# Optimization experiments

Measured on AMD Instinct MI355X. Metric: run time of the kernel, lower is better.

## Reference

```python
import jax, jax.numpy as jnp
import numpy as np

N = 100000
E = 1600000
D_IN = 128
D_H = 256


def setup_inputs() -> dict:
    key = jax.random.key(0)
    ks = jax.random.split(key, 8)
    x = jax.random.normal(ks[0], (N, D_IN), dtype=jnp.float32)
    x_tilde = jax.random.normal(ks[1], (N, D_IN), dtype=jnp.float32)
    adj_row = jnp.sort(jax.random.randint(ks[2], (E,), 0, N, dtype=jnp.int32))
    adj_col = jax.random.randint(ks[3], (E,), 0, N, dtype=jnp.int32)
    # normalized-ish positive edge weights
    adj_vals = jax.random.uniform(ks[4], (E,), dtype=jnp.float32) / 16.0
    # Linear weight (torch layout [out, in]), xavier-ish scale
    W1 = jax.random.normal(ks[5], (D_H, D_IN), dtype=jnp.float32) * (2.0 / (D_IN + D_H)) ** 0.5
    prelu_a = jnp.full((1,), 0.25, dtype=jnp.float32)  # PReLU default slope
    w_bil = jax.random.normal(ks[6], (D_H, D_H), dtype=jnp.float32) * (2.0 / (2 * D_H)) ** 0.5
    return {"x": x, "x_tilde": x_tilde, "adj_vals": adj_vals, "adj_row": adj_row,
            "adj_col": adj_col, "W1": W1, "prelu_a": prelu_a, "w_bil": w_bil}


def reference(x, x_tilde, adj_vals, adj_row, adj_col, W1, prelu_a, w_bil):
    n = x.shape[0]

    def gcn(feat):
        # SpMM: agg[r] = sum_e vals[e] * feat[col[e]] for edges with row[e]==r
        gathered = adj_vals[:, None] * feat[adj_col]  # [E, D_IN]
        agg = jax.ops.segment_sum(gathered, adj_row, num_segments=n)  # [N, D_IN]
        z = agg @ W1.T  # [N, D_H]
        return jnp.where(z >= 0, z, prelu_a[0] * z)  # PReLU

    h = gcn(x)
    h_tilde = gcn(x_tilde)
    s = jax.nn.sigmoid(jnp.mean(h, axis=0))  # [D_H] readout (same for every row)
    dp = jnp.einsum('ni,ij,j->n', h, w_bil, s)  # bilinear discriminator
    dn = jnp.einsum('ni,ij,j->n', h_tilde, w_bil, s)
    return jnp.concatenate([dp, dn])[None, :]  # [1, 2N]
```

## Files before the change

kernel.cpp:

```cpp
#include <hip/hip_runtime.h>


__device__ __forceinline__ float b2f(unsigned short s) {
    union { unsigned int u; float f; } c; c.u = ((unsigned int)s) << 16; return c.f;
}
__device__ __forceinline__ unsigned short f2b(float f) {
    union { float f; unsigned int u; } c; c.f = f;
    unsigned int u = c.u;
    unsigned int r = u + 0x7FFFu + ((u >> 16) & 1u);
    return (unsigned short)(r >> 16);
}
__device__ __forceinline__ unsigned int pack2(float lo, float hi) {
    return ((unsigned int)f2b(hi) << 16) | f2b(lo);
}
__device__ __forceinline__ void fma8(float* a, float v, uint4 w) {
    a[0] = fmaf(v, b2f((unsigned short)w.x), a[0]);
    a[1] = fmaf(v, b2f((unsigned short)(w.x >> 16)), a[1]);
    a[2] = fmaf(v, b2f((unsigned short)w.y), a[2]);
    a[3] = fmaf(v, b2f((unsigned short)(w.y >> 16)), a[3]);
    a[4] = fmaf(v, b2f((unsigned short)w.z), a[4]);
    a[5] = fmaf(v, b2f((unsigned short)(w.z >> 16)), a[5]);
    a[6] = fmaf(v, b2f((unsigned short)w.w), a[6]);
    a[7] = fmaf(v, b2f((unsigned short)(w.w >> 16)), a[7]);
}

typedef __attribute__((ext_vector_type(8))) short bf16x8;
typedef __attribute__((ext_vector_type(4))) float f32x4;

#define T_TILES 10

__global__ __launch_bounds__(256) void prep(
    const int* __restrict__ row, int* __restrict__ rp, int n, int e, int rb,
    const float* __restrict__ w1, unsigned short* __restrict__ w1b, int pb,
    const float* __restrict__ x, const float* __restrict__ xt,
    unsigned short* __restrict__ xint, int total8, int halfcb)
{
    int b = blockIdx.x, tid = threadIdx.x;
    if (b < rb) {
        int i = b * 256 + tid;
        if (i > e) return;
        if (i == 0) {
            int r1 = row[0];
            for (int rr = 0; rr <= r1; ++rr) rp[rr] = 0;
        } else if (i == e) {
            int r0 = row[e - 1];
            for (int rr = r0 + 1; rr <= n; ++rr) rp[rr] = e;
        } else {
            int r0 = row[i - 1], r1 = row[i];
            for (int rr = r0 + 1; rr <= r1; ++rr) rp[rr] = i;
        }
    } else if (b < rb + pb) {
        int i = (b - rb) * 256 + tid;
        if (i < 32768) w1b[i] = f2b(w1[i]);
    } else {
        int cb = b - rb - pb;
        int which = (cb >= halfcb) ? 1 : 0;
        int i = (cb - which * halfcb) * 256 + tid;
        if (i >= total8) return;
        const float* s = which ? xt : x;
        int node = i >> 4, sub = i & 15;
        const float4* p = (const float4*)s + (size_t)i * 2;
        float4 a = p[0], bb = p[1];
        uint4 o;
        o.x = pack2(a.x, a.y);  o.y = pack2(a.z, a.w);
        o.z = pack2(bb.x, bb.y); o.w = pack2(bb.z, bb.w);
        *(uint4*)(xint + (size_t)node * 256 + which * 128 + sub * 8) = o;
    }
}

__global__ __launch_bounds__(256) void spmm_dual4(
    const unsigned short* __restrict__ xint, const float* __restrict__ vals,
    const int* __restrict__ col, const int* __restrict__ row_ptr,
    unsigned short* __restrict__ aggx, unsigned short* __restrict__ aggt, int n)
{
    int wave = threadIdx.x >> 6;
    int lane = threadIdx.x & 63;
    int g = lane >> 4, l = lane & 15;
    int r = blockIdx.x * 4 + wave;
    if (r >= n) return;
    int e0 = row_ptr[r], e1 = row_ptr[r + 1];
    float ax[8], at[8];
#pragma unroll
    for (int d = 0; d < 8; ++d) { ax[d] = 0.f; at[d] = 0.f; }
    for (int chunk = e0; chunk < e1; chunk += 64) {
        int m = e1 - chunk; if (m > 64) m = 64;
        int ce = chunk + (lane < m ? lane : m - 1);
        int cc = col[ce];
        float cv = (lane < m) ? vals[ce] : 0.f;
        for (int base = 0; base < m; base += 16) {
            uint4 xw[4], tw[4];
            float fv[4];
#pragma unroll
            for (int u = 0; u < 4; ++u) {
                int idx = base + 4 * u + g;
                int idc = idx < m ? idx : m - 1;
                int c  = __shfl(cc, idc, 64);
                float v = __shfl(cv, idc, 64);
                fv[u] = (idx < m) ? v : 0.f;
                const uint4* p = (const uint4*)(xint + (size_t)c * 256);
                xw[u] = p[l];
                tw[u] = p[16 + l];
            }
#pragma unroll
            for (int u = 0; u < 4; ++u) { fma8(ax, fv[u], xw[u]); fma8(at, fv[u], tw[u]); }
        }
    }
#pragma unroll
    for (int d = 0; d < 8; ++d) {
        ax[d] += __shfl_xor(ax[d], 16, 64);
        ax[d] += __shfl_xor(ax[d], 32, 64);
        at[d] += __shfl_xor(at[d], 16, 64);
        at[d] += __shfl_xor(at[d], 32, 64);
    }
    if (g == 0) {
        uint4 o;
        o.x = pack2(ax[0], ax[1]); o.y = pack2(ax[2], ax[3]);
        o.z = pack2(ax[4], ax[5]); o.w = pack2(ax[6], ax[7]);
        ((uint4*)(aggx + (size_t)r * 128))[l] = o;
    } else if (g == 1) {
        uint4 o;
        o.x = pack2(at[0], at[1]); o.y = pack2(at[2], at[3]);
        o.z = pack2(at[4], at[5]); o.w = pack2(at[6], at[7]);
        ((uint4*)(aggt + (size_t)r * 128))[l] = o;
    }
}

__global__ __launch_bounds__(256) void gemm_colsum3(
    const short* __restrict__ aggb, const short* __restrict__ w1,
    const float* __restrict__ pa, float* __restrict__ partial, int ntiles, int nb)
{
    int tid = threadIdx.x;
    int w = tid >> 6, lane = tid & 63;
    int nl = lane & 15, quad = lane >> 4;
    const short* brow = w1 + ((size_t)(4 * w) * 16 + nl) * 128 + quad * 8;
    bf16x8 bf[4][4];
#pragma unroll
    for (int j = 0; j < 4; ++j)
#pragma unroll
        for (int k = 0; k < 4; ++k)
            bf[j][k] = *(const bf16x8*)(brow + j * 2048 + k * 32);
    float aslope = pa[0];
    float cs[4] = {0.f, 0.f, 0.f, 0.f};
    int t0 = blockIdx.x * T_TILES;
    int nt = ntiles - t0; if (nt > T_TILES) nt = T_TILES;
    for (int i = 0; i < nt; ++i) {
        const short* arow = aggb + ((size_t)(t0 + i) * 16 + nl) * 128 + quad * 8;
        bf16x8 af[4];
#pragma unroll
        for (int k = 0; k < 4; ++k) af[k] = *(const bf16x8*)(arow + k * 32);
        f32x4 acc[4];
#pragma unroll
        for (int j = 0; j < 4; ++j) acc[j] = (f32x4){0.f, 0.f, 0.f, 0.f};
#pragma unroll
        for (int k = 0; k < 4; ++k)
#pragma unroll
            for (int j = 0; j < 4; ++j)
                acc[j] = __builtin_amdgcn_mfma_f32_16x16x32_bf16(af[k], bf[j][k], acc[j], 0, 0, 0);
#pragma unroll
        for (int j = 0; j < 4; ++j)
#pragma unroll
            for (int r = 0; r < 4; ++r) {
                float z = acc[j][r];
                cs[j] += (z >= 0.f) ? z : aslope * z;
            }
    }
#pragma unroll
    for (int j = 0; j < 4; ++j) {
        cs[j] += __shfl_xor(cs[j], 16, 64);
        cs[j] += __shfl_xor(cs[j], 32, 64);
    }
    if (quad == 0)
#pragma unroll
        for (int j = 0; j < 4; ++j)
            partial[(size_t)((4 * w + j) * 16 + nl) * nb + blockIdx.x] = cs[j];
}

__global__ __launch_bounds__(256) void reduce_sig(
    const float* __restrict__ partial, int nb, float* __restrict__ s_out, float invN)
{
    __shared__ float l[256];
    int d = blockIdx.x, tid = threadIdx.x;
    float s = 0.f;
    for (int i = tid; i < nb; i += 256)
        s += partial[(size_t)d * nb + i];
    l[tid] = s;
    __syncthreads();
    for (int o = 128; o > 0; o >>= 1) {
        if (tid < o) l[tid] += l[tid + o];
        __syncthreads();
    }
    if (tid == 0) s_out[d] = 1.f / (1.f + expf(-l[0] * invN));
}

__global__ __launch_bounds__(256) void compute_v(
    const float* __restrict__ s_in, const float* __restrict__ wbil,
    float* __restrict__ v)
{
    __shared__ float s_lds[256];
    int t = threadIdx.x;
    s_lds[t] = s_in[t];
    __syncthreads();
    const float* wrow = wbil + (size_t)t * 256;
    float acc = 0.f;
#pragma unroll 8
    for (int j = 0; j < 256; ++j)
        acc = fmaf(wrow[j], s_lds[j], acc);
    v[t] = acc;
}

__global__ __launch_bounds__(256) void gemm_dp2(
    const short* __restrict__ aggx, const short* __restrict__ aggt,
    const short* __restrict__ w1, const float* __restrict__ pa,
    const float* __restrict__ v, float* __restrict__ out, int ntiles, int N)
{
    __shared__ float dpbuf[4][T_TILES * 16];
    int tid = threadIdx.x;
    int w = tid >> 6, lane = tid & 63;
    int nl = lane & 15, quad = lane >> 4;
    const short* agg = blockIdx.y ? aggt : aggx;
    const short* brow = w1 + ((size_t)(4 * w) * 16 + nl) * 128 + quad * 8;
    bf16x8 bf[4][4];
#pragma unroll
    for (int j = 0; j < 4; ++j)
#pragma unroll
        for (int k = 0; k < 4; ++k)
            bf[j][k] = *(const bf16x8*)(brow + j * 2048 + k * 32);
    float vreg[4];
#pragma unroll
    for (int j = 0; j < 4; ++j) vreg[j] = v[(4 * w + j) * 16 + nl];
    float aslope = pa[0];
    int t0 = blockIdx.x * T_TILES;
    int nt = ntiles - t0; if (nt > T_TILES) nt = T_TILES;
    for (int i = 0; i < nt; ++i) {
        const short* arow = agg + ((size_t)(t0 + i) * 16 + nl) * 128 + quad * 8;
        bf16x8 af[4];
#pragma unroll
        for (int k = 0; k < 4; ++k) af[k] = *(const bf16x8*)(arow + k * 32);
        f32x4 acc[4];
#pragma unroll
        for (int j = 0; j < 4; ++j) acc[j] = (f32x4){0.f, 0.f, 0.f, 0.f};
#pragma unroll
        for (int k = 0; k < 4; ++k)
#pragma unroll
            for (int j = 0; j < 4; ++j)
                acc[j] = __builtin_amdgcn_mfma_f32_16x16x32_bf16(af[k], bf[j][k], acc[j], 0, 0, 0);
        float p[4] = {0.f, 0.f, 0.f, 0.f};
#pragma unroll
        for (int j = 0; j < 4; ++j)
#pragma unroll
            for (int r = 0; r < 4; ++r) {
                float z = acc[j][r];
                float h = (z >= 0.f) ? z : aslope * z;
                p[r] = fmaf(h, vreg[j], p[r]);
            }
#pragma unroll
        for (int r = 0; r < 4; ++r) {
            p[r] += __shfl_xor(p[r], 1, 64);
            p[r] += __shfl_xor(p[r], 2, 64);
            p[r] += __shfl_xor(p[r], 4, 64);
            p[r] += __shfl_xor(p[r], 8, 64);
        }
        if (nl == 0)
#pragma unroll
            for (int r = 0; r < 4; ++r)
                dpbuf[w][i * 16 + quad * 4 + r] = p[r];
    }
    __syncthreads();
    int nloc = nt * 16;
    for (int idx = tid; idx < nloc; idx += 256) {
        float s = dpbuf[0][idx] + dpbuf[1][idx] + dpbuf[2][idx] + dpbuf[3][idx];
        out[(size_t)blockIdx.y * N + (size_t)t0 * 16 + idx] = s;
    }
}

extern "C" void kernel_launch(void* const* d_in, const int* in_sizes, int n_in,
                              void* d_out, int out_size, void* d_ws, size_t ws_size,
                              hipStream_t stream) {
    const float* x    = (const float*)d_in[0];
    const float* xt   = (const float*)d_in[1];
    const float* vals = (const float*)d_in[2];
    const int* row    = (const int*)d_in[3];
    const int* col    = (const int*)d_in[4];
    const float* w1   = (const float*)d_in[5];
    const float* pa   = (const float*)d_in[6];
    const float* wb   = (const float*)d_in[7];

    const int N = in_sizes[0] / 128;
    const int E = in_sizes[2];
    const int ntiles = (N + 15) / 16;
    const int cs_blocks = (ntiles + T_TILES - 1) / T_TILES;

    char* ws = (char*)d_ws;
    size_t off = 0;
    auto alloc = [&](size_t bytes) { char* p = ws + off; off = (off + bytes + 255) & ~(size_t)255; return p; };
    int* row_ptr         = (int*)alloc((size_t)(N + 1) * 4);
    unsigned short* aggx = (unsigned short*)alloc((size_t)N * 128 * 2);
    unsigned short* aggt = (unsigned short*)alloc((size_t)N * 128 * 2);
    unsigned short* w1b  = (unsigned short*)alloc(32768 * 2);
    float* partial       = (float*)alloc((size_t)cs_blocks * 256 * 4);
    float* svec          = (float*)alloc(256 * 4);
    float* vvec          = (float*)alloc(256 * 4);
    unsigned short* xint = (unsigned short*)alloc((size_t)N * 256 * 2);

    int rb = (E + 1 + 255) / 256;
    int pb = 128;
    int total8 = (N * 128) / 8;
    int halfcb = (total8 + 255) / 256;
    prep<<<rb + pb + 2 * halfcb, 256, 0, stream>>>(
        row, row_ptr, N, E, rb, w1, w1b, pb, x, xt, xint, total8, halfcb);

    spmm_dual4<<<(N + 3) / 4, 256, 0, stream>>>(xint, vals, col, row_ptr, aggx, aggt, N);

    gemm_colsum3<<<cs_blocks, 256, 0, stream>>>(
        (const short*)aggx, (const short*)w1b, pa, partial, ntiles, cs_blocks);
    reduce_sig<<<256, 256, 0, stream>>>(partial, cs_blocks, svec, 1.0f / (float)N);
    compute_v<<<1, 256, 0, stream>>>(svec, wb, vvec);
    gemm_dp2<<<dim3(cs_blocks, 2), 256, 0, stream>>>(
        (const short*)aggx, (const short*)aggt, (const short*)w1b, pa, vvec,
        (float*)d_out, ntiles, N);
}
```

Before: 337.2 us.

## Fuse sigmoid readout with bilinear vector via grid barrier; merge dp passes

Merges reduce_sig and compute_v into one kernel: each of the 256 blocks writes its sigmoid entry, then all blocks wait on a global atomic counter (zeroed in prep) before computing one element of v. This removes a single-block launch. The discriminator GEMM now handles both x and x_tilde in one block, reusing the W1 fragments in registers, and T_TILES is halved to keep the grid size similar. The bf16 conversion in prep now packs 16 elements per thread instead of 8. The spin barrier relies on all 256 blocks being co-resident, which holds on this GPU but is not guaranteed in general.

```diff
diff --git a/kernel.cpp b/kernel.cpp
--- a/kernel.cpp
+++ b/kernel.cpp
@@ -27,15 +27,21 @@
 typedef __attribute__((ext_vector_type(8))) short bf16x8;
 typedef __attribute__((ext_vector_type(4))) float f32x4;
 
-#define T_TILES 10
+#define T_TILES 5
 
 __global__ __launch_bounds__(256) void prep(
     const int* __restrict__ row, int* __restrict__ rp, int n, int e, int rb,
     const float* __restrict__ w1, unsigned short* __restrict__ w1b, int pb,
     const float* __restrict__ x, const float* __restrict__ xt,
-    unsigned short* __restrict__ xint, int total8, int halfcb)
+    unsigned short* __restrict__ xint, int total16, int halfcb,
+    unsigned int* __restrict__ done)
 {
     int b = blockIdx.x, tid = threadIdx.x;
+    int zb = rb + pb + 2 * halfcb;
+    if (b == zb) {
+        if (tid == 0) *done = 0u;
+        return;
+    }
     if (b < rb) {
         int i = b * 256 + tid;
         if (i > e) return;
@@ -55,16 +61,20 @@
     } else {
         int cb = b - rb - pb;
         int which = (cb >= halfcb) ? 1 : 0;
-        int i = (cb - which * halfcb) * 256 + tid;
-        if (i >= total8) return;
+        int j = (cb - which * halfcb) * 256 + tid;
+        if (j >= total16) return;
         const float* s = which ? xt : x;
-        int node = i >> 4, sub = i & 15;
-        const float4* p = (const float4*)s + (size_t)i * 2;
-        float4 a = p[0], bb = p[1];
-        uint4 o;
-        o.x = pack2(a.x, a.y);  o.y = pack2(a.z, a.w);
-        o.z = pack2(bb.x, bb.y); o.w = pack2(bb.z, bb.w);
-        *(uint4*)(xint + (size_t)node * 256 + which * 128 + sub * 8) = o;
+        int node = j >> 3, sub16 = j & 7;
+        const float4* p = (const float4*)s + (size_t)j * 4;
+        float4 a0 = p[0], a1 = p[1], a2 = p[2], a3 = p[3];
+        uint4 o0, o1;
+        o0.x = pack2(a0.x, a0.y);  o0.y = pack2(a0.z, a0.w);
+        o0.z = pack2(a1.x, a1.y);  o0.w = pack2(a1.z, a1.w);
+        o1.x = pack2(a2.x, a2.y);  o1.y = pack2(a2.z, a2.w);
+        o1.z = pack2(a3.x, a3.y);  o1.w = pack2(a3.z, a3.w);
+        unsigned short* dst = xint + (size_t)node * 256 + which * 128 + sub16 * 16;
+        *(uint4*)(dst) = o0;
+        *(uint4*)(dst + 8) = o1;
     }
 }
 
@@ -175,8 +185,10 @@
             partial[(size_t)((4 * w + j) * 16 + nl) * nb + blockIdx.x] = cs[j];
 }
 
-__global__ __launch_bounds__(256) void reduce_sig(
-    const float* __restrict__ partial, int nb, float* __restrict__ s_out, float invN)
+__global__ __launch_bounds__(256) void sigv_fused(
+    const float* __restrict__ partial, int nb, const float* __restrict__ wbil,
+    float* __restrict__ svec, unsigned int* __restrict__ done,
+    float* __restrict__ v, float invN)
 {
     __shared__ float l[256];
     int d = blockIdx.x, tid = threadIdx.x;
@@ -189,26 +201,25 @@
         if (tid < o) l[tid] += l[tid + o];
         __syncthreads();
     }
-    if (tid == 0) s_out[d] = 1.f / (1.f + expf(-l[0] * invN));
-}
-
-__global__ __launch_bounds__(256) void compute_v(
-    const float* __restrict__ s_in, const float* __restrict__ wbil,
-    float* __restrict__ v)
-{
-    __shared__ float s_lds[256];
-    int t = threadIdx.x;
-    s_lds[t] = s_in[t];
+    if (tid == 0) {
+        float sv = 1.f / (1.f + __expf(-l[0] * invN));
+        __hip_atomic_store(&svec[d], sv, __ATOMIC_RELEASE, __HIP_MEMORY_SCOPE_AGENT);
+        __hip_atomic_fetch_add(done, 1u, __ATOMIC_RELEASE, __HIP_MEMORY_SCOPE_AGENT);
+        while (__hip_atomic_load(done, __ATOMIC_ACQUIRE, __HIP_MEMORY_SCOPE_AGENT) < 256u)
+            __builtin_amdgcn_s_sleep(1);
+    }
     __syncthreads();
-    const float* wrow = wbil + (size_t)t * 256;
-    float acc = 0.f;
-#pragma unroll 8
-    for (int j = 0; j < 256; ++j)
-        acc = fmaf(wrow[j], s_lds[j], acc);
-    v[t] = acc;
-}
-
-__global__ __launch_bounds__(256) void gemm_dp2(
+    float sj = __hip_atomic_load(&svec[tid], __ATOMIC_ACQUIRE, __HIP_MEMORY_SCOPE_AGENT);
+    l[tid] = wbil[(size_t)d * 256 + tid] * sj;
+    __syncthreads();
+    for (int o = 128; o > 0; o >>= 1) {
+        if (tid < o) l[tid] += l[tid + o];
+        __syncthreads();
+    }
+    if (tid == 0) v[d] = l[0];
+}
+
+__global__ __launch_bounds__(256) void gemm_dp_both(
     const short* __restrict__ aggx, const short* __restrict__ aggt,
     const short* __restrict__ w1, const float* __restrict__ pa,
     const float* __restrict__ v, float* __restrict__ out, int ntiles, int N)
@@ -217,7 +228,6 @@
     int tid = threadIdx.x;
     int w = tid >> 6, lane = tid & 63;
     int nl = lane & 15, quad = lane >> 4;
-    const short* agg = blockIdx.y ? aggt : aggx;
     const short* brow = w1 + ((size_t)(4 * w) * 16 + nl) * 128 + quad * 8;
     bf16x8 bf[4][4];
 #pragma unroll
@@ -231,45 +241,49 @@
     float aslope = pa[0];
     int t0 = blockIdx.x * T_TILES;
     int nt = ntiles - t0; if (nt > T_TILES) nt = T_TILES;
-    for (int i = 0; i < nt; ++i) {
-        const short* arow = agg + ((size_t)(t0 + i) * 16 + nl) * 128 + quad * 8;
-        bf16x8 af[4];
-#pragma unroll
-        for (int k = 0; k < 4; ++k) af[k] = *(const bf16x8*)(arow + k * 32);
-        f32x4 acc[4];
-#pragma unroll
-        for (int j = 0; j < 4; ++j) acc[j] = (f32x4){0.f, 0.f, 0.f, 0.f};
-#pragma unroll
-        for (int k = 0; k < 4; ++k)
+    for (int mat = 0; mat < 2; ++mat) {
+        const short* agg = mat ? aggt : aggx;
+        for (int i = 0; i < nt; ++i) {
+            const short* arow = agg + ((size_t)(t0 + i) * 16 + nl) * 128 + quad * 8;
+            bf16x8 af[4];
+#pragma unroll
+            for (int k = 0; k < 4; ++k) af[k] = *(const bf16x8*)(arow + k * 32);
+            f32x4 acc[4];
+#pragma unroll
+            for (int j = 0; j < 4; ++j) acc[j] = (f32x4){0.f, 0.f, 0.f, 0.f};
+#pragma unroll
+            for (int k = 0; k < 4; ++k)
+#pragma unroll
+                for (int j = 0; j < 4; ++j)
+                    acc[j] = __builtin_amdgcn_mfma_f32_16x16x32_bf16(af[k], bf[j][k], acc[j], 0, 0, 0);
+            float p[4] = {0.f, 0.f, 0.f, 0.f};
 #pragma unroll
             for (int j = 0; j < 4; ++j)
-                acc[j] = __builtin_amdgcn_mfma_f32_16x16x32_bf16(af[k], bf[j][k], acc[j], 0, 0, 0);
-        float p[4] = {0.f, 0.f, 0.f, 0.f};
-#pragma unroll
-        for (int j = 0; j < 4; ++j)
+#pragma unroll
+                for (int r = 0; r < 4; ++r) {
+                    float z = acc[j][r];
+                    float h = (z >= 0.f) ? z : aslope * z;
+                    p[r] = fmaf(h, vreg[j], p[r]);
+                }
 #pragma unroll
             for (int r = 0; r < 4; ++r) {
-                float z = acc[j][r];
-                float h = (z >= 0.f) ? z : aslope * z;
-                p[r] = fmaf(h, vreg[j], p[r]);
+                p[r] += __shfl_xor(p[r], 1, 64);
+                p[r] += __shfl_xor(p[r], 2, 64);
+                p[r] += __shfl_xor(p[r], 4, 64);
+                p[r] += __shfl_xor(p[r], 8, 64);
             }
-#pragma unroll
-        for (int r = 0; r < 4; ++r) {
-            p[r] += __shfl_xor(p[r], 1, 64);
-            p[r] += __shfl_xor(p[r], 2, 64);
-            p[r] += __shfl_xor(p[r], 4, 64);
-            p[r] += __shfl_xor(p[r], 8, 64);
+            if (nl == 0)
+#pragma unroll
+                for (int r = 0; r < 4; ++r)
+                    dpbuf[w][i * 16 + quad * 4 + r] = p[r];
         }
-        if (nl == 0)
-#pragma unroll
-            for (int r = 0; r < 4; ++r)
-                dpbuf[w][i * 16 + quad * 4 + r] = p[r];
-    }
-    __syncthreads();
-    int nloc = nt * 16;
-    for (int idx = tid; idx < nloc; idx += 256) {
-        float s = dpbuf[0][idx] + dpbuf[1][idx] + dpbuf[2][idx] + dpbuf[3][idx];
-        out[(size_t)blockIdx.y * N + (size_t)t0 * 16 + idx] = s;
+        __syncthreads();
+        int nloc = nt * 16;
+        for (int idx = tid; idx < nloc; idx += 256) {
+            float s = dpbuf[0][idx] + dpbuf[1][idx] + dpbuf[2][idx] + dpbuf[3][idx];
+            out[(size_t)mat * N + (size_t)t0 * 16 + idx] = s;
+        }
+        __syncthreads();
     }
 }
 
@@ -300,22 +314,25 @@
     float* partial       = (float*)alloc((size_t)cs_blocks * 256 * 4);
     float* svec          = (float*)alloc(256 * 4);
     float* vvec          = (float*)alloc(256 * 4);
+    unsigned int* done   = (unsigned int*)alloc(256);
     unsigned short* xint = (unsigned short*)alloc((size_t)N * 256 * 2);
 
     int rb = (E + 1 + 255) / 256;
     int pb = 128;
-    int total8 = (N * 128) / 8;
-    int halfcb = (total8 + 255) / 256;
-    prep<<<rb + pb + 2 * halfcb, 256, 0, stream>>>(
-        row, row_ptr, N, E, rb, w1, w1b, pb, x, xt, xint, total8, halfcb);
+    int total16 = (N * 128) / 16;
+    int halfcb = (total16 + 255) / 256;
+    prep<<<rb + pb + 2 * halfcb + 1, 256, 0, stream>>>(
+        row, row_ptr, N, E, rb, w1, w1b, pb, x, xt, xint, total16, halfcb, done);
 
     spmm_dual4<<<(N + 3) / 4, 256, 0, stream>>>(xint, vals, col, row_ptr, aggx, aggt, N);
 
     gemm_colsum3<<<cs_blocks, 256, 0, stream>>>(
         (const short*)aggx, (const short*)w1b, pa, partial, ntiles, cs_blocks);
-    reduce_sig<<<256, 256, 0, stream>>>(partial, cs_blocks, svec, 1.0f / (float)N);
-    compute_v<<<1, 256, 0, stream>>>(svec, wb, vvec);
-    gemm_dp2<<<dim3(cs_blocks, 2), 256, 0, stream>>>(
+
+    sigv_fused<<<256, 256, 0, stream>>>(
+        partial, cs_blocks, wb, svec, done, vvec, 1.0f / (float)N);
+
+    gemm_dp_both<<<cs_blocks, 256, 0, stream>>>(
         (const short*)aggx, (const short*)aggt, (const short*)w1b, pa, vvec,
         (float*)d_out, ntiles, N);
 }
```

Measured after the change: 351.3 us. 1.04x slower.
